# Kernel tuning notes

Measured on AMD Instinct MI355X. Metric: run time of the kernel, lower is better.

Reference implementation:

```python
import jax, jax.numpy as jnp
import numpy as np

# pywt 'db4' analysis filters (dec_lo, dec_hi)
DEC_LO = np.array([-0.010597401784997278, 0.032883011666982945, 0.030841381835986965,
                   -0.18703481171888114, -0.02798376941698385, 0.6308807679295904,
                   0.7148465705525415, 0.23037781330885523], dtype=np.float32)
DEC_HI = np.array([-0.23037781330885523, 0.7148465705525415, -0.6308807679295904,
                   -0.02798376941698385, 0.18703481171888114, 0.030841381835986965,
                   -0.032883011666982945, -0.010597401784997278], dtype=np.float32)
J = 3          # dwt levels for subwindow_size=64 with db4
DWT_LEN = 84   # 14 (lo) + 35 + 21 + 14 (his)
NEG_SLOPE = 1e-3
FILT = np.stack([DEC_LO[::-1].copy(), DEC_HI[::-1].copy()])[:, None, :]  # [2,1,8] reversed, as in pytorch_wavelets


def _afb1d(x):
    # Single-level analysis filter bank along last axis, reflect padding (pytorch_wavelets mode='reflect')
    N = x.shape[-1]
    L = 8
    outsize = (N + L - 1) // 2
    p = 2 * (outsize - 1) - N + L
    xp = jnp.pad(x, [(0, 0)] * (x.ndim - 1) + [(p // 2, (p + 1) // 2)], mode='reflect')
    lead = x.shape[:-1]
    xr = xp.reshape((-1, 1, xp.shape[-1]))
    out = jax.lax.conv_general_dilated(xr, jnp.asarray(FILT, dtype=x.dtype), (2,), 'VALID')  # [B,2,outsize]
    lo = out[:, 0].reshape(lead + (outsize,))
    hi = out[:, 1].reshape(lead + (outsize,))
    return lo, hi


def _dwt(x):
    # J-level DWT; returns concat([lo_J, hi_1, ..., hi_J], axis=-1), matching [x_lo]+x_hi cat order
    his = []
    lo = x
    for _ in range(J):
        lo, hi = _afb1d(lo)
        his.append(hi)
    return jnp.concatenate([lo] + his, axis=-1)


def setup_inputs() -> dict:
    key = jax.random.key(0)
    k1, k2, k3 = jax.random.split(key, 3)
    B, K = 16384, 16
    x = jax.random.normal(k1, (B, 1, 64, 8, 8), dtype=jnp.float32)
    conv_w = jax.random.normal(k2, (K, 1, DWT_LEN, 8, 8), dtype=jnp.float32) * (1.0 / np.sqrt(DWT_LEN * 64))
    conv_b = jax.random.normal(k3, (K,), dtype=jnp.float32) * 0.01
    return {"x": x, "conv_w": conv_w, "conv_b": conv_b}


def reference(x, conv_w, conv_b):
    # x: [B,1,T=64,8,8]; time_interval=1, no maxpool, subwindow_nbins=1 (subwindow = full window)
    xt = jnp.moveaxis(x, 2, -1)            # [B,1,8,8,T] -> DWT along time
    d = _dwt(xt)                           # [B,1,8,8,DWT_LEN]
    d = jnp.moveaxis(d, -1, 2)             # [B,1,DWT_LEN,8,8]
    # Conv3d with kernel spanning full [DWT_LEN,8,8] == full contraction -> [B,K]
    feat = jnp.einsum('bcdhw,kcdhw->bk', d, conv_w) + conv_b
    # Dropout3d is identity in eval; LeakyReLU(0.001) then flatten (already [B, nbins*K], nbins=1)
    return jnp.where(feat >= 0, feat, NEG_SLOPE * feat)
```

## Files before the change

kernel.cpp:

```cpp
#include <hip/hip_runtime.h>
#include <hip/hip_bf16.h>

#define DWT_LEN_C 84
#define TDIM 64
#define INNER 4096
#define KOUT 16
#define KSPLIT 2
#define HCOLS 2048
#define OITER 16

typedef __attribute__((ext_vector_type(8))) short short8;
typedef __attribute__((ext_vector_type(4))) float floatx4;

__device__ __forceinline__ unsigned short bf16_rne(float f) {
    unsigned u = __float_as_uint(f);
    unsigned r = u + 0x7fffu + ((u >> 16) & 1u);
    return (unsigned short)(r >> 16);
}

__device__ const float c_dec_lo[8] = {-0.010597401784997278f, 0.032883011666982945f, 0.030841381835986965f,
                                      -0.18703481171888114f, -0.02798376941698385f, 0.6308807679295904f,
                                      0.7148465705525415f, 0.23037781330885523f};
__device__ const float c_dec_hi[8] = {-0.23037781330885523f, 0.7148465705525415f, -0.6308807679295904f,
                                      -0.02798376941698385f, 0.18703481171888114f, 0.030841381835986965f,
                                      -0.032883011666982945f, -0.010597401784997278f};

__device__ void afb1d_col(const float* v, int N, float* lo, float* hi, int M) {
    for (int i = 0; i < M; ++i) {
        float slo = 0.f, shi = 0.f;
        for (int j = 0; j < 8; ++j) {
            int idx = 2 * i + j - 6;
            if (idx < 0) idx = -idx;
            if (idx >= N) idx = 2 * N - 2 - idx;
            float c = v[idx];
            slo = fmaf(c, c_dec_lo[7 - j], slo);
            shi = fmaf(c, c_dec_hi[7 - j], shi);
        }
        lo[i] = slo; hi[i] = shi;
    }
}

__global__ __launch_bounds__(256) void build_weff_bf16(const float* __restrict__ conv_w,
                                                       unsigned short* __restrict__ Wb) {
    __shared__ float Wd[DWT_LEN_C][TDIM];
    const int t0 = threadIdx.x;
    if (t0 < TDIM) {
        float v[64];
        for (int n = 0; n < 64; ++n) v[n] = (n == t0) ? 1.f : 0.f;
        float lo1[35], hi1[35], lo2[21], hi2[21], lo3[14], hi3[14];
        afb1d_col(v, 64, lo1, hi1, 35);
        afb1d_col(lo1, 35, lo2, hi2, 21);
        afb1d_col(lo2, 21, lo3, hi3, 14);
        for (int i = 0; i < 14; ++i) Wd[i][t0] = lo3[i];
        for (int i = 0; i < 35; ++i) Wd[14 + i][t0] = hi1[i];
        for (int i = 0; i < 21; ++i) Wd[49 + i][t0] = hi2[i];
        for (int i = 0; i < 14; ++i) Wd[70 + i][t0] = hi3[i];
    }
    __syncthreads();

    const int idx = blockIdx.x * 256 + threadIdx.x;
    const int k = idx >> 12;
    const int col = idx & 4095;
    const int t = col >> 6;
    const int hw = col & 63;
    float s = 0.f;
    const float* cw = conv_w + (size_t)k * DWT_LEN_C * 64 + hw;
#pragma unroll 4
    for (int dd = 0; dd < DWT_LEN_C; ++dd)
        s = fmaf(cw[dd * 64], Wd[dd][t], s);
    Wb[idx] = bf16_rne(s);
}

__global__ __launch_bounds__(256) void dwt_mfma(const float* __restrict__ x,
                                                const unsigned short* __restrict__ Wb,
                                                float* __restrict__ partial, int B) {
    __shared__ __align__(16) unsigned short Wlds[KOUT * HCOLS];
    const int t = threadIdx.x;
    const int rowgroup = blockIdx.x >> 1;
    const int kh = blockIdx.x & 1;

    {
        const int n = t & 15;
        const int c0 = (t >> 4) * 128;
        const unsigned short* src = Wb + n * INNER + kh * HCOLS + c0;
#pragma unroll
        for (int g = 0; g < 16; ++g) {
            const int c = c0 + g * 8;
            *(short8*)&Wlds[n * HCOLS + (c ^ ((n & 7) * 8))] = *(const short8*)(src + g * 8);
        }
    }
    __syncthreads();

    const int lane = t & 63;
    const int wid = t >> 6;
    const int qg = lane >> 4;
    const int mrow = lane & 15;
    const int rowbase = rowgroup * 64 + wid * 16;
    const float* xrow = x + (size_t)(rowbase + mrow) * INNER + kh * HCOLS + qg * 8;
    const unsigned short* wrow = &Wlds[mrow * HCOLS];
    const int swz = (mrow & 7) * 8;

    floatx4 acc = {0.f, 0.f, 0.f, 0.f};
    float4 bufA[8], bufB[8];

#define XLOAD(buf, it)                                                          \
    {                                                                           \
        const float* p = xrow + (it) * 128;                                     \
        _Pragma("unroll")                                                       \
        for (int s = 0; s < 4; ++s) {                                           \
            buf[2 * s]     = *(const float4*)(p + s * 32);                      \
            buf[2 * s + 1] = *(const float4*)(p + s * 32 + 4);                  \
        }                                                                       \
    }

#define XCOMPUTE(buf, it)                                                       \
    {                                                                           \
        _Pragma("unroll")                                                       \
        for (int s = 0; s < 4; ++s) {                                           \
            const float4 lo = buf[2 * s];                                       \
            const float4 hi = buf[2 * s + 1];                                   \
            short8 a;                                                           \
            a[0] = (short)bf16_rne(lo.x); a[1] = (short)bf16_rne(lo.y);         \
            a[2] = (short)bf16_rne(lo.z); a[3] = (short)bf16_rne(lo.w);         \
            a[4] = (short)bf16_rne(hi.x); a[5] = (short)bf16_rne(hi.y);         \
            a[6] = (short)bf16_rne(hi.z); a[7] = (short)bf16_rne(hi.w);         \
            const int col = (it) * 128 + s * 32 + qg * 8;                       \
            const short8 b = *(const short8*)(wrow + (col ^ swz));              \
            acc = __builtin_amdgcn_mfma_f32_16x16x32_bf16(a, b, acc, 0, 0, 0);  \
        }                                                                       \
    }

    XLOAD(bufA, 0);
#pragma unroll 1
    for (int it = 0; it < OITER; it += 2) {
        XLOAD(bufB, it + 1);
        XCOMPUTE(bufA, it);
        if (it + 2 < OITER) XLOAD(bufA, it + 2);
        XCOMPUTE(bufB, it + 1);
    }
#undef XLOAD
#undef XCOMPUTE

    const int orow = rowbase + qg * 4;
    float* pq = partial + (size_t)kh * B * KOUT;
#pragma unroll
    for (int r = 0; r < 4; ++r)
        pq[(size_t)(orow + r) * KOUT + mrow] = acc[r];
}

__global__ __launch_bounds__(256) void finish(const float* __restrict__ partial,
                                              const float* __restrict__ bias,
                                              float* __restrict__ out, int B) {
    const int idx4 = (blockIdx.x * 256 + threadIdx.x) * 4;
    if (idx4 >= B * KOUT) return;
    const size_t stride = (size_t)B * KOUT;
    float4 s = *(const float4*)(partial + idx4);
#pragma unroll
    for (int q = 1; q < KSPLIT; ++q) {
        float4 p = *(const float4*)(partial + q * stride + idx4);
        s.x += p.x; s.y += p.y; s.z += p.z; s.w += p.w;
    }
    const float4 bb = *(const float4*)(bias + (idx4 & 15));
    s.x += bb.x; s.y += bb.y; s.z += bb.z; s.w += bb.w;
    s.x = (s.x >= 0.f) ? s.x : 1e-3f * s.x;
    s.y = (s.y >= 0.f) ? s.y : 1e-3f * s.y;
    s.z = (s.z >= 0.f) ? s.z : 1e-3f * s.z;
    s.w = (s.w >= 0.f) ? s.w : 1e-3f * s.w;
    *(float4*)(out + idx4) = s;
}

extern "C" void kernel_launch(void* const* d_in, const int* in_sizes, int n_in,
                              void* d_out, int out_size, void* d_ws, size_t ws_size,
                              hipStream_t stream) {
    const float* x      = (const float*)d_in[0];
    const float* conv_w = (const float*)d_in[1];
    const float* conv_b = (const float*)d_in[2];
    float* out = (float*)d_out;
    const int B = in_sizes[0] / INNER;

    float* partial = (float*)d_ws;
    unsigned short* Wb = (unsigned short*)((char*)d_ws + ((size_t)4 << 20));

    build_weff_bf16<<<(KOUT * INNER) / 256, 256, 0, stream>>>(conv_w, Wb);
    dwt_mfma<<<(B / 64) * KSPLIT, 256, 0, stream>>>(x, Wb, partial, B);
    finish<<<(B * KOUT / 4 + 255) / 256, 256, 0, stream>>>(partial, conv_b, out, B);
}
```

Before: 57.49 us.

## Fuse K-split reduction and bias/LeakyReLU epilogue into MFMA kernel via LDS

Each block now runs 512 threads: two groups of four waves each handle one half of the 4096-wide contraction for the same 64 rows. Both weight halves are staged in LDS. The two partial sums are combined through LDS, and bias plus LeakyReLU are applied in the same kernel. This removes the partial-sum buffer round trip through global memory and the separate finish launch. In exchange, LDS per block doubles to 128KB, which may limit occupancy, and a block barrier is added before the epilogue.

```diff
diff --git a/kernel.cpp b/kernel.cpp
--- a/kernel.cpp
+++ b/kernel.cpp
@@ -5,7 +5,6 @@
 #define TDIM 64
 #define INNER 4096
 #define KOUT 16
-#define KSPLIT 2
 #define HCOLS 2048
 #define OITER 16
 
@@ -71,33 +70,37 @@
     Wb[idx] = bf16_rne(s);
 }
 
-__global__ __launch_bounds__(256) void dwt_mfma(const float* __restrict__ x,
-                                                const unsigned short* __restrict__ Wb,
-                                                float* __restrict__ partial, int B) {
-    __shared__ __align__(16) unsigned short Wlds[KOUT * HCOLS];
+__global__ __launch_bounds__(512, 2) void dwt_mfma_fused(const float* __restrict__ x,
+                                                         const unsigned short* __restrict__ Wb,
+                                                         const float* __restrict__ bias,
+                                                         float* __restrict__ out, int B) {
+    __shared__ __align__(16) unsigned short Wlds[2][KOUT * HCOLS];
     const int t = threadIdx.x;
-    const int rowgroup = blockIdx.x >> 1;
-    const int kh = blockIdx.x & 1;
+    const int rowgroup = blockIdx.x;
 
     {
-        const int n = t & 15;
-        const int c0 = (t >> 4) * 128;
-        const unsigned short* src = Wb + n * INNER + kh * HCOLS + c0;
+        const int half = t >> 8;
+        const int u = t & 255;
+        const int n = u & 15;
+        const int c0 = (u >> 4) * 128;
+        const unsigned short* src = Wb + n * INNER + half * HCOLS + c0;
 #pragma unroll
         for (int g = 0; g < 16; ++g) {
             const int c = c0 + g * 8;
-            *(short8*)&Wlds[n * HCOLS + (c ^ ((n & 7) * 8))] = *(const short8*)(src + g * 8);
+            *(short8*)&Wlds[half][n * HCOLS + (c ^ ((n & 7) * 8))] = *(const short8*)(src + g * 8);
         }
     }
     __syncthreads();
 
     const int lane = t & 63;
     const int wid = t >> 6;
+    const int kh = wid >> 2;
+    const int w4 = wid & 3;
     const int qg = lane >> 4;
     const int mrow = lane & 15;
-    const int rowbase = rowgroup * 64 + wid * 16;
+    const int rowbase = rowgroup * 64 + w4 * 16;
     const float* xrow = x + (size_t)(rowbase + mrow) * INNER + kh * HCOLS + qg * 8;
-    const unsigned short* wrow = &Wlds[mrow * HCOLS];
+    const unsigned short* wrow = &Wlds[kh][mrow * HCOLS];
     const int swz = (mrow & 7) * 8;
 
     floatx4 acc = {0.f, 0.f, 0.f, 0.f};
@@ -141,32 +144,23 @@
 #undef XLOAD
 #undef XCOMPUTE
 
-    const int orow = rowbase + qg * 4;
-    float* pq = partial + (size_t)kh * B * KOUT;
+    __syncthreads();
+    float* red = (float*)&Wlds[0][0];
+    if (kh == 1)
+        *(float4*)&red[(w4 * 64 + lane) * 4] = *(float4*)&acc;
+    __syncthreads();
+    if (kh == 0) {
+        const float4 o = *(const float4*)&red[(w4 * 64 + lane) * 4];
+        acc[0] += o.x; acc[1] += o.y; acc[2] += o.z; acc[3] += o.w;
+        const float bv = bias[mrow];
+        const int orow = rowbase + qg * 4;
 #pragma unroll
-    for (int r = 0; r < 4; ++r)
-        pq[(size_t)(orow + r) * KOUT + mrow] = acc[r];
-}
-
-__global__ __launch_bounds__(256) void finish(const float* __restrict__ partial,
-                                              const float* __restrict__ bias,
-                                              float* __restrict__ out, int B) {
-    const int idx4 = (blockIdx.x * 256 + threadIdx.x) * 4;
-    if (idx4 >= B * KOUT) return;
-    const size_t stride = (size_t)B * KOUT;
-    float4 s = *(const float4*)(partial + idx4);
-#pragma unroll
-    for (int q = 1; q < KSPLIT; ++q) {
-        float4 p = *(const float4*)(partial + q * stride + idx4);
-        s.x += p.x; s.y += p.y; s.z += p.z; s.w += p.w;
+        for (int r = 0; r < 4; ++r) {
+            float val = acc[r] + bv;
+            val = (val >= 0.f) ? val : 1e-3f * val;
+            out[(size_t)(orow + r) * KOUT + mrow] = val;
+        }
     }
-    const float4 bb = *(const float4*)(bias + (idx4 & 15));
-    s.x += bb.x; s.y += bb.y; s.z += bb.z; s.w += bb.w;
-    s.x = (s.x >= 0.f) ? s.x : 1e-3f * s.x;
-    s.y = (s.y >= 0.f) ? s.y : 1e-3f * s.y;
-    s.z = (s.z >= 0.f) ? s.z : 1e-3f * s.z;
-    s.w = (s.w >= 0.f) ? s.w : 1e-3f * s.w;
-    *(float4*)(out + idx4) = s;
 }
 
 extern "C" void kernel_launch(void* const* d_in, const int* in_sizes, int n_in,
@@ -178,10 +172,8 @@
     float* out = (float*)d_out;
     const int B = in_sizes[0] / INNER;
 
-    float* partial = (float*)d_ws;
-    unsigned short* Wb = (unsigned short*)((char*)d_ws + ((size_t)4 << 20));
+    unsigned short* Wb = (unsigned short*)d_ws;
 
     build_weff_bf16<<<(KOUT * INNER) / 256, 256, 0, stream>>>(conv_w, Wb);
-    dwt_mfma<<<(B / 64) * KSPLIT, 256, 0, stream>>>(x, Wb, partial, B);
-    finish<<<(B * KOUT / 4 + 255) / 256, 256, 0, stream>>>(partial, conv_b, out, B);
+    dwt_mfma_fused<<<B / 64, 512, 0, stream>>>(x, Wb, conv_b, out, B);
 }
```

Measured after the change: 63.55 us. 1.11x slower.

## Split GEMM reduction four ways and use packed bf16 conversion

Applied to the files above, without the earlier changes.

The inner dimension is now split into four quarters instead of two. This halves the LDS weight tile per block, doubles the grid, and allows a launch-bounds occupancy hint of 4 blocks per CU. Scalar bf16 rounding of the activations is replaced by the packed float2-to-bfloat162 intrinsic, which may map to a hardware conversion instruction. In exchange the partial-sum buffer doubles, so the finish kernel reads more, and each block has a shorter pipelined loop with weight-load overhead that is amortized over less work.

```diff
diff --git a/kernel.cpp b/kernel.cpp
--- a/kernel.cpp
+++ b/kernel.cpp
@@ -5,9 +5,9 @@
 #define TDIM 64
 #define INNER 4096
 #define KOUT 16
-#define KSPLIT 2
-#define HCOLS 2048
-#define OITER 16
+#define KSPLIT 4
+#define QCOLS 1024
+#define OITER 8
 
 typedef __attribute__((ext_vector_type(8))) short short8;
 typedef __attribute__((ext_vector_type(4))) float floatx4;
@@ -71,22 +71,22 @@
     Wb[idx] = bf16_rne(s);
 }
 
-__global__ __launch_bounds__(256) void dwt_mfma(const float* __restrict__ x,
-                                                const unsigned short* __restrict__ Wb,
-                                                float* __restrict__ partial, int B) {
-    __shared__ __align__(16) unsigned short Wlds[KOUT * HCOLS];
+__global__ __launch_bounds__(256, 4) void dwt_mfma(const float* __restrict__ x,
+                                                   const unsigned short* __restrict__ Wb,
+                                                   float* __restrict__ partial, int B) {
+    __shared__ __align__(16) unsigned short Wlds[KOUT * QCOLS];
     const int t = threadIdx.x;
-    const int rowgroup = blockIdx.x >> 1;
-    const int kh = blockIdx.x & 1;
+    const int rowgroup = blockIdx.x >> 2;
+    const int kq = blockIdx.x & 3;
 
     {
         const int n = t & 15;
-        const int c0 = (t >> 4) * 128;
-        const unsigned short* src = Wb + n * INNER + kh * HCOLS + c0;
+        const int c0 = (t >> 4) * 64;
+        const unsigned short* src = Wb + n * INNER + kq * QCOLS + c0;
 #pragma unroll
-        for (int g = 0; g < 16; ++g) {
+        for (int g = 0; g < 8; ++g) {
             const int c = c0 + g * 8;
-            *(short8*)&Wlds[n * HCOLS + (c ^ ((n & 7) * 8))] = *(const short8*)(src + g * 8);
+            *(short8*)&Wlds[n * QCOLS + (c ^ ((n & 7) * 8))] = *(const short8*)(src + g * 8);
         }
     }
     __syncthreads();
@@ -96,8 +96,8 @@
     const int qg = lane >> 4;
     const int mrow = lane & 15;
     const int rowbase = rowgroup * 64 + wid * 16;
-    const float* xrow = x + (size_t)(rowbase + mrow) * INNER + kh * HCOLS + qg * 8;
-    const unsigned short* wrow = &Wlds[mrow * HCOLS];
+    const float* xrow = x + (size_t)(rowbase + mrow) * INNER + kq * QCOLS + qg * 8;
+    const unsigned short* wrow = &Wlds[mrow * QCOLS];
     const int swz = (mrow & 7) * 8;
 
     floatx4 acc = {0.f, 0.f, 0.f, 0.f};
@@ -119,14 +119,14 @@
         for (int s = 0; s < 4; ++s) {                                           \
             const float4 lo = buf[2 * s];                                       \
             const float4 hi = buf[2 * s + 1];                                   \
-            short8 a;                                                           \
-            a[0] = (short)bf16_rne(lo.x); a[1] = (short)bf16_rne(lo.y);         \
-            a[2] = (short)bf16_rne(lo.z); a[3] = (short)bf16_rne(lo.w);         \
-            a[4] = (short)bf16_rne(hi.x); a[5] = (short)bf16_rne(hi.y);         \
-            a[6] = (short)bf16_rne(hi.z); a[7] = (short)bf16_rne(hi.w);         \
+            union { __hip_bfloat162 h[4]; short8 s8; } cv;                      \
+            cv.h[0] = __float22bfloat162_rn(float2{lo.x, lo.y});                \
+            cv.h[1] = __float22bfloat162_rn(float2{lo.z, lo.w});                \
+            cv.h[2] = __float22bfloat162_rn(float2{hi.x, hi.y});                \
+            cv.h[3] = __float22bfloat162_rn(float2{hi.z, hi.w});                \
             const int col = (it) * 128 + s * 32 + qg * 8;                       \
             const short8 b = *(const short8*)(wrow + (col ^ swz));              \
-            acc = __builtin_amdgcn_mfma_f32_16x16x32_bf16(a, b, acc, 0, 0, 0);  \
+            acc = __builtin_amdgcn_mfma_f32_16x16x32_bf16(cv.s8, b, acc, 0, 0, 0); \
         }                                                                       \
     }
 
@@ -142,7 +142,7 @@
 #undef XCOMPUTE
 
     const int orow = rowbase + qg * 4;
-    float* pq = partial + (size_t)kh * B * KOUT;
+    float* pq = partial + (size_t)kq * B * KOUT;
 #pragma unroll
     for (int r = 0; r < 4; ++r)
         pq[(size_t)(orow + r) * KOUT + mrow] = acc[r];
@@ -179,7 +179,7 @@
     const int B = in_sizes[0] / INNER;
 
     float* partial = (float*)d_ws;
-    unsigned short* Wb = (unsigned short*)((char*)d_ws + ((size_t)4 << 20));
+    unsigned short* Wb = (unsigned short*)((char*)d_ws + ((size_t)8 << 20));
 
     build_weff_bf16<<<(KOUT * INNER) / 256, 256, 0, stream>>>(conv_w, Wb);
     dwt_mfma<<<(B / 64) * KSPLIT, 256, 0, stream>>>(x, Wb, partial, B);
```

Measured after the change: 60.30 us. 1.05x slower.
